# Performance work log

Measured on AMD Instinct MI355X. Metric: run time of the kernel, lower is better.

The kernel has to match this reference:

```python
import jax, jax.numpy as jnp
import numpy as np

HALF = 24576          # per-side HalfKP features (64 king sq * 6 piece * 64 sq)
NUMEL = 2 * HALF      # util.half_kp_numel()
BASE = 128
B = 8192


def _linear(x, W, b):
    return x @ W.T + b


def setup_inputs() -> dict:
    key = jax.random.key(0)
    ks = jax.random.split(key, 16)
    s = 0.01
    return {
        "pov": jax.random.uniform(ks[0], (B, 1), dtype=jnp.float32),
        "white": jax.random.uniform(ks[1], (B, HALF), dtype=jnp.float32),
        "black": jax.random.uniform(ks[2], (B, HALF), dtype=jnp.float32),
        "w_aff_W": jax.random.normal(ks[3], (BASE, NUMEL), dtype=jnp.float32) * s,
        "w_aff_b": jax.random.normal(ks[4], (BASE,), dtype=jnp.float32) * s,
        "b_aff_W": jax.random.normal(ks[5], (BASE, NUMEL), dtype=jnp.float32) * s,
        "b_aff_b": jax.random.normal(ks[6], (BASE,), dtype=jnp.float32) * s,
        "fc0_W": jax.random.normal(ks[7], (32, 2 * BASE), dtype=jnp.float32) * s,
        "fc0_b": jax.random.normal(ks[8], (32,), dtype=jnp.float32) * s,
        "fc1_W": jax.random.normal(ks[9], (32, 32), dtype=jnp.float32) * s,
        "fc1_b": jax.random.normal(ks[10], (32,), dtype=jnp.float32) * s,
        "fc2_W": jax.random.normal(ks[11], (32, 64), dtype=jnp.float32) * s,
        "fc2_b": jax.random.normal(ks[12], (32,), dtype=jnp.float32) * s,
        "fc3_W": jax.random.normal(ks[13], (1, 96), dtype=jnp.float32) * s,
        "fc3_b": jax.random.normal(ks[14], (1,), dtype=jnp.float32) * s,
    }


def reference(pov, white, black, w_aff_W, w_aff_b, b_aff_W, b_aff_b,
              fc0_W, fc0_b, fc1_W, fc1_b, fc2_W, fc2_b, fc3_W, fc3_b):
    # util.half_kp(a, b) = cat([a, b], dim=1)
    w_feat = jnp.concatenate([white, black], axis=1)  # [B, NUMEL]
    b_feat = jnp.concatenate([black, white], axis=1)
    w_ = _linear(w_feat, w_aff_W, w_aff_b)            # [B, 128]
    b_ = _linear(b_feat, b_aff_W, b_aff_b)
    wb = jnp.concatenate([w_, b_], axis=1)            # [B, 256]
    bw = jnp.concatenate([b_, w_], axis=1)
    base = jax.nn.relu(pov * wb + (1.0 - pov) * bw)
    x = jax.nn.relu(_linear(base, fc0_W, fc0_b))      # [B, 32]
    x = jnp.concatenate([x, jax.nn.relu(_linear(x, fc1_W, fc1_b))], axis=1)  # [B, 64]
    x = jnp.concatenate([x, jax.nn.relu(_linear(x, fc2_W, fc2_b))], axis=1)  # [B, 96]
    return _linear(x, fc3_W, fc3_b)                   # [B, 1]
```

## Files before the change

kernel.cpp:

```cpp
#include <hip/hip_runtime.h>
#include <hip/hip_bf16.h>
#include <stdint.h>

typedef float f32x4 __attribute__((ext_vector_type(4)));
typedef float fvec4 __attribute__((ext_vector_type(4)));
typedef short bf16x8 __attribute__((ext_vector_type(8)));
typedef short bf16x4 __attribute__((ext_vector_type(4)));

#define HALF_K 24576
#define NUMELK 49152
#define BATCH  8192
#define BM 256
#define BN 256
#define BK 64

__device__ __forceinline__ short f2bf(float f) {
  __hip_bfloat16 h = __float2bfloat16(f);
  return __builtin_bit_cast(short, h);
}

__device__ __forceinline__ void gload_lds16(const short* g, short* l) {
  __builtin_amdgcn_global_load_lds(
      (const __attribute__((address_space(1))) unsigned*)g,
      (__attribute__((address_space(3))) unsigned*)l, 16, 0, 0);
}

__global__ __launch_bounds__(256)
void nnue_prep(const float* __restrict__ wW, const float* __restrict__ bW,
               short* __restrict__ Bprep) {
  int gid = blockIdx.x * 256 + threadIdx.x;
  int KT  = gid >> 11;
  int rem = gid & 2047;
  int col = rem >> 3;
  int kc  = rem & 7;
  int kg  = KT * 64 + kc * 8;
  const float* src;
  if (col < 128) {
    src = wW + (size_t)col * NUMELK + kg;
  } else {
    int kk = (kg < HALF_K) ? (kg + HALF_K) : (kg - HALF_K);
    src = bW + (size_t)(col - 128) * NUMELK + kk;
  }
  fvec4 v0 = ((const fvec4*)src)[0];
  fvec4 v1 = ((const fvec4*)src)[1];
  bf16x8 o;
  o[0] = f2bf(v0[0]); o[1] = f2bf(v0[1]); o[2] = f2bf(v0[2]); o[3] = f2bf(v0[3]);
  o[4] = f2bf(v1[0]); o[5] = f2bf(v1[1]); o[6] = f2bf(v1[2]); o[7] = f2bf(v1[3]);
  *(bf16x8*)(Bprep + (size_t)KT * 16384 + col * 64 + ((kc ^ (col & 7)) << 3)) = o;
}

__global__ __launch_bounds__(512, 1)
void nnue_gemm(const float* __restrict__ white, const float* __restrict__ black,
               const short* __restrict__ Bprep, float* __restrict__ partial,
               int kchunk, int S) {
  __shared__ short Alds[2][BM * BK];
  __shared__ short Blds[2][BN * BK];

  const int t    = threadIdx.x;
  const int lane = t & 63;
  const int wid  = t >> 6;

  const int bid = blockIdx.x;
  const int xcd = bid & 7, i = bid >> 3;
  const int xpk = 8 / S;
  const int ks  = xcd / xpk;
  const int mt  = (xcd % xpk) * (32 / xpk) + i;
  const int m0  = mt * BM;
  const int k0  = ks * kchunk;
  const int KT0 = k0 / BK;

  f32x4 acc[8][4];
  const f32x4 zero = {0.f, 0.f, 0.f, 0.f};
#pragma unroll
  for (int a = 0; a < 8; ++a)
#pragma unroll
    for (int b = 0; b < 4; ++b) acc[a][b] = zero;

  const int wm = wid >> 2, wn = wid & 3;
  const int l15 = lane & 15, l4 = lane >> 4;

  const int rbase = t >> 4;
  const int cchunk = t & 15;
  const size_t a_off = (size_t)(m0 + rbase) * HALF_K + cchunk * 4;
  const int swz = ((cchunk >> 1) ^ (rbase & 7)) << 3;
  const int halfsh = (cchunk & 1) * 4;

  fvec4 va[8];

  auto issueA = [&](int kg) {
    const float* A; int ka;
    if (kg < HALF_K) { A = white; ka = kg; } else { A = black; ka = kg - HALF_K; }
    const float* base = A + a_off + ka;
#pragma unroll
    for (int j = 0; j < 8; ++j)
      va[j] = *(const fvec4*)(base + (size_t)32 * j * HALF_K);
  };

  auto issueB = [&](int kt_glob, int buf) {
    const short* src = Bprep + (size_t)kt_glob * (BN * BK) + wid * 2048 + lane * 8;
    short* dst = &Blds[buf][wid * 2048];
#pragma unroll
    for (int j = 0; j < 4; ++j)
      gload_lds16(src + j * 512, dst + j * 512);
  };

  auto writeA = [&](int buf) {
#pragma unroll
    for (int j = 0; j < 8; ++j) {
      int row = 32 * j + rbase;
      bf16x4 o;
      o[0] = f2bf(va[j][0]); o[1] = f2bf(va[j][1]);
      o[2] = f2bf(va[j][2]); o[3] = f2bf(va[j][3]);
      *(bf16x4*)&Alds[buf][row * 64 + swz + halfsh] = o;
    }
  };

  const int niter = kchunk / BK;

  issueB(KT0, 0);
  issueA(k0);
  writeA(0);
  __syncthreads();

  for (int kt = 0; kt < niter; ++kt) {
    const int cur = kt & 1;
    const bool hn = (kt + 1 < niter);
    if (hn) {
      issueB(KT0 + kt + 1, cur ^ 1);
      issueA(k0 + (kt + 1) * BK);
    }

    const short* Ab = Alds[cur];
    const short* Bb = Blds[cur];
#pragma unroll
    for (int kstep = 0; kstep < 2; ++kstep) {
      const int kc = kstep * 4 + l4;
      bf16x8 bfr[4];
#pragma unroll
      for (int nf = 0; nf < 4; ++nf) {
        int col = wn * 64 + nf * 16 + l15;
        bfr[nf] = *(const bf16x8*)&Bb[col * 64 + ((kc ^ (col & 7)) << 3)];
      }
#pragma unroll
      for (int mf = 0; mf < 8; ++mf) {
        int row = wm * 128 + mf * 16 + l15;
        bf16x8 af = *(const bf16x8*)&Ab[row * 64 + ((kc ^ (row & 7)) << 3)];
#pragma unroll
        for (int nf = 0; nf < 4; ++nf)
          acc[mf][nf] = __builtin_amdgcn_mfma_f32_16x16x32_bf16(af, bfr[nf], acc[mf][nf], 0, 0, 0);
      }
    }

    if (hn) writeA(cur ^ 1);
    __syncthreads();
  }

  float* P = partial + ((size_t)ks * BATCH + m0) * 256;
#pragma unroll
  for (int mf = 0; mf < 8; ++mf) {
    int row = wm * 128 + mf * 16 + l4 * 4;
#pragma unroll
    for (int nf = 0; nf < 4; ++nf) {
      int col = wn * 64 + nf * 16 + l15;
#pragma unroll
      for (int rr = 0; rr < 4; ++rr)
        P[(size_t)(row + rr) * 256 + col] = acc[mf][nf][rr];
    }
  }
}

__global__ __launch_bounds__(256)
void nnue_tail(const float* __restrict__ partial, int S,
               const float* __restrict__ pov,
               const float* __restrict__ waffb, const float* __restrict__ baffb,
               const float* __restrict__ fc0W, const float* __restrict__ fc0b,
               const float* __restrict__ fc1W, const float* __restrict__ fc1b,
               const float* __restrict__ fc2W, const float* __restrict__ fc2b,
               const float* __restrict__ fc3W, const float* __restrict__ fc3b,
               float* __restrict__ out) {
  __shared__ float w0s[32 * 256];
  __shared__ float w1s[32 * 32];
  __shared__ float w2s[32 * 64];
  __shared__ float w3s[96];
  __shared__ float b0s[32], b1s[32], b2s[32];
  __shared__ float base_s[4][256];
  __shared__ float b3s;

  const int t = threadIdx.x;
  for (int i = t; i < 8192; i += 256) { int j = i >> 8, k = i & 255; w0s[(j << 8) | ((k + j) & 255)] = fc0W[i]; }
  for (int i = t; i < 1024; i += 256) { int j = i >> 5, k = i & 31;  w1s[(j << 5) | ((k + j) & 31)]  = fc1W[i]; }
  for (int i = t; i < 2048; i += 256) { int j = i >> 6, k = i & 63;  w2s[(j << 6) | ((k + j) & 63)]  = fc2W[i]; }
  if (t < 96) w3s[t] = fc3W[t];
  if (t < 32) { b0s[t] = fc0b[t]; b1s[t] = fc1b[t]; b2s[t] = fc2b[t]; }
  if (t == 0) b3s = fc3b[0];
  __syncthreads();

  const int wid = t >> 6, lane = t & 63;
  const int m = blockIdx.x * 4 + wid;
  const float pv = pov[m];

  float val[4];
  {
    const float* p = partial + (size_t)m * 256 + lane * 4;
    fvec4 a = *(const fvec4*)p;
    for (int s = 1; s < S; ++s) a += *(const fvec4*)(p + (size_t)s * BATCH * 256);
    const int c0 = lane * 4;
#pragma unroll
    for (int j = 0; j < 4; ++j) {
      int c = c0 + j;
      float bias = (c < 128) ? waffb[c] : baffb[c - 128];
      val[j] = a[j] + bias;
    }
  }
#pragma unroll
  for (int j = 0; j < 4; ++j) {
    float other = __shfl(val[j], lane ^ 32, 64);
    if (lane < 32) {
      int c = lane * 4 + j;
      float w = val[j], b = other;
      base_s[wid][c]       = fmaxf(pv * w + (1.f - pv) * b, 0.f);
      base_s[wid][c + 128] = fmaxf(pv * b + (1.f - pv) * w, 0.f);
    }
  }
  __syncthreads();

  const int j = lane & 31, half = lane >> 5;
  const float* bs = &base_s[wid][0];

  float s0 = 0.f;
  for (int k = 0; k < 128; ++k) {
    int kk = half * 128 + k;
    s0 += bs[kk] * w0s[(j << 8) | ((kk + j) & 255)];
  }
  s0 += __shfl(s0, lane ^ 32, 64);
  float x0 = fmaxf(s0 + b0s[j], 0.f);

  float s1 = 0.f;
  for (int k = 0; k < 32; ++k)
    s1 += __shfl(x0, k, 64) * w1s[(j << 5) | ((k + j) & 31)];
  float x1 = fmaxf(s1 + b1s[j], 0.f);

  float s2 = 0.f;
  for (int k = 0; k < 32; ++k) {
    s2 += __shfl(x0, k, 64) * w2s[(j << 6) | ((k + j) & 63)];
    s2 += __shfl(x1, k, 64) * w2s[(j << 6) | ((k + 32 + j) & 63)];
  }
  float x2 = fmaxf(s2 + b2s[j], 0.f);

  float s3 = 0.f;
  for (int k = 0; k < 32; ++k) {
    s3 += __shfl(x0, k, 64) * w3s[k];
    s3 += __shfl(x1, k, 64) * w3s[32 + k];
    s3 += __shfl(x2, k, 64) * w3s[64 + k];
  }
  if (lane == 0) out[m] = s3 + b3s;
}

extern "C" void kernel_launch(void* const* d_in, const int* in_sizes, int n_in,
                              void* d_out, int out_size, void* d_ws, size_t ws_size,
                              hipStream_t stream) {
  const float* pov   = (const float*)d_in[0];
  const float* white = (const float*)d_in[1];
  const float* black = (const float*)d_in[2];
  const float* wW    = (const float*)d_in[3];
  const float* wb    = (const float*)d_in[4];
  const float* bW    = (const float*)d_in[5];
  const float* bb    = (const float*)d_in[6];
  const float* fc0W  = (const float*)d_in[7];
  const float* fc0b  = (const float*)d_in[8];
  const float* fc1W  = (const float*)d_in[9];
  const float* fc1b  = (const float*)d_in[10];
  const float* fc2W  = (const float*)d_in[11];
  const float* fc2b  = (const float*)d_in[12];
  const float* fc3W  = (const float*)d_in[13];
  const float* fc3b  = (const float*)d_in[14];
  float* out = (float*)d_out;

  short* Bprep = (short*)d_ws;
  const size_t BWS_BYTES = (size_t)256 * NUMELK * 2;
  float* partial = (float*)((char*)d_ws + BWS_BYTES);
  const size_t PART1 = (size_t)BATCH * 256 * 4;

  int S = 8;
  if (ws_size < BWS_BYTES + 8 * PART1) S = 4;
  if (ws_size < BWS_BYTES + 4 * PART1) S = 2;
  if (ws_size < BWS_BYTES + 2 * PART1) S = 1;

  nnue_prep<<<dim3(6144), 256, 0, stream>>>(wW, bW, Bprep);
  nnue_gemm<<<dim3(32 * S), 512, 0, stream>>>(white, black, Bprep, partial, NUMELK / S, S);
  nnue_tail<<<dim3(BATCH / 4), 256, 0, stream>>>(partial, S, pov, wb, bb,
      fc0W, fc0b, fc1W, fc1b, fc2W, fc2b, fc3W, fc3b, out);
}
```

Measured before the change: 447.1 us.

## Halve GEMM M-tile and restructure pipeline with manual waitcnt and barriers

Shrinks the GEMM M tile from 256 to 128 rows and doubles the grid, so more workgroups are resident per CU. LDS is reorganised to a double-buffered A tile and a single-buffered B tile. The usual __syncthreads are replaced by hand-placed s_waitcnt, s_barrier, sched_barrier and s_setprio, so the next A global loads overlap the MFMA work. In exchange the B weights are re-read by twice as many blocks. The vmcnt accounting is delicate: the global_load_lds traffic for B may not be fully waited on before B is used, which risks a race.

```diff
diff --git a/kernel.cpp b/kernel.cpp
--- a/kernel.cpp
+++ b/kernel.cpp
@@ -10,7 +10,7 @@
 #define HALF_K 24576
 #define NUMELK 49152
 #define BATCH  8192
-#define BM 256
+#define BM 128
 #define BN 256
 #define BK 64
 
@@ -49,89 +49,74 @@
   *(bf16x8*)(Bprep + (size_t)KT * 16384 + col * 64 + ((kc ^ (col & 7)) << 3)) = o;
 }
 
-__global__ __launch_bounds__(512, 1)
+__global__ __launch_bounds__(512, 4)
 void nnue_gemm(const float* __restrict__ white, const float* __restrict__ black,
                const short* __restrict__ Bprep, float* __restrict__ partial,
                int kchunk, int S) {
-  __shared__ short Alds[2][BM * BK];
-  __shared__ short Blds[2][BN * BK];
+  __shared__ short A0s[BM * BK];
+  __shared__ short A1s[BM * BK];
+  __shared__ short Bls[BN * BK];
 
   const int t    = threadIdx.x;
   const int lane = t & 63;
   const int wid  = t >> 6;
 
   const int bid = blockIdx.x;
-  const int xcd = bid & 7, i = bid >> 3;
+  const int xcd = bid & 7, bi = bid >> 3;
   const int xpk = 8 / S;
   const int ks  = xcd / xpk;
-  const int mt  = (xcd % xpk) * (32 / xpk) + i;
+  const int mt  = (xcd % xpk) * (64 / xpk) + bi;
   const int m0  = mt * BM;
   const int k0  = ks * kchunk;
   const int KT0 = k0 / BK;
 
-  f32x4 acc[8][4];
+  f32x4 acc[4][4];
   const f32x4 zero = {0.f, 0.f, 0.f, 0.f};
 #pragma unroll
-  for (int a = 0; a < 8; ++a)
+  for (int a = 0; a < 4; ++a)
 #pragma unroll
     for (int b = 0; b < 4; ++b) acc[a][b] = zero;
 
   const int wm = wid >> 2, wn = wid & 3;
   const int l15 = lane & 15, l4 = lane >> 4;
 
-  const int rbase = t >> 4;
+  const int rbase  = t >> 4;
   const int cchunk = t & 15;
   const size_t a_off = (size_t)(m0 + rbase) * HALF_K + cchunk * 4;
-  const int swz = ((cchunk >> 1) ^ (rbase & 7)) << 3;
+  const int swz    = ((cchunk >> 1) ^ (rbase & 7)) << 3;
   const int halfsh = (cchunk & 1) * 4;
 
-  fvec4 va[8];
+  fvec4 va[4];
 
   auto issueA = [&](int kg) {
-    const float* A; int ka;
-    if (kg < HALF_K) { A = white; ka = kg; } else { A = black; ka = kg - HALF_K; }
-    const float* base = A + a_off + ka;
-#pragma unroll
-    for (int j = 0; j < 8; ++j)
+    const float* Af; int ka;
+    if (kg < HALF_K) { Af = white; ka = kg; } else { Af = black; ka = kg - HALF_K; }
+    const float* base = Af + a_off + ka;
+#pragma unroll
+    for (int j = 0; j < 4; ++j)
       va[j] = *(const fvec4*)(base + (size_t)32 * j * HALF_K);
   };
 
-  auto issueB = [&](int kt_glob, int buf) {
-    const short* src = Bprep + (size_t)kt_glob * (BN * BK) + wid * 2048 + lane * 8;
-    short* dst = &Blds[buf][wid * 2048];
+  auto issueB = [&](int KT) {
+    const short* src = Bprep + (size_t)KT * 16384 + wid * 2048 + lane * 8;
+    short* dst = &Bls[wid * 2048];
 #pragma unroll
     for (int j = 0; j < 4; ++j)
       gload_lds16(src + j * 512, dst + j * 512);
   };
 
-  auto writeA = [&](int buf) {
-#pragma unroll
-    for (int j = 0; j < 8; ++j) {
+  auto writeA = [&](short* Ad) {
+#pragma unroll
+    for (int j = 0; j < 4; ++j) {
       int row = 32 * j + rbase;
       bf16x4 o;
       o[0] = f2bf(va[j][0]); o[1] = f2bf(va[j][1]);
       o[2] = f2bf(va[j][2]); o[3] = f2bf(va[j][3]);
-      *(bf16x4*)&Alds[buf][row * 64 + swz + halfsh] = o;
+      *(bf16x4*)&Ad[row * 64 + swz + halfsh] = o;
     }
   };
 
-  const int niter = kchunk / BK;
-
-  issueB(KT0, 0);
-  issueA(k0);
-  writeA(0);
-  __syncthreads();
-
-  for (int kt = 0; kt < niter; ++kt) {
-    const int cur = kt & 1;
-    const bool hn = (kt + 1 < niter);
-    if (hn) {
-      issueB(KT0 + kt + 1, cur ^ 1);
-      issueA(k0 + (kt + 1) * BK);
-    }
-
-    const short* Ab = Alds[cur];
-    const short* Bb = Blds[cur];
+  auto compute = [&](const short* Ab) {
 #pragma unroll
     for (int kstep = 0; kstep < 2; ++kstep) {
       const int kc = kstep * 4 + l4;
@@ -139,26 +124,58 @@
 #pragma unroll
       for (int nf = 0; nf < 4; ++nf) {
         int col = wn * 64 + nf * 16 + l15;
-        bfr[nf] = *(const bf16x8*)&Bb[col * 64 + ((kc ^ (col & 7)) << 3)];
+        bfr[nf] = *(const bf16x8*)&Bls[col * 64 + ((kc ^ (col & 7)) << 3)];
       }
 #pragma unroll
-      for (int mf = 0; mf < 8; ++mf) {
-        int row = wm * 128 + mf * 16 + l15;
+      for (int mf = 0; mf < 4; ++mf) {
+        int row = wm * 64 + mf * 16 + l15;
         bf16x8 af = *(const bf16x8*)&Ab[row * 64 + ((kc ^ (row & 7)) << 3)];
 #pragma unroll
         for (int nf = 0; nf < 4; ++nf)
           acc[mf][nf] = __builtin_amdgcn_mfma_f32_16x16x32_bf16(af, bfr[nf], acc[mf][nf], 0, 0, 0);
       }
     }
-
-    if (hn) writeA(cur ^ 1);
-    __syncthreads();
+  };
+
+  const int niter = kchunk / BK;
+
+  issueA(k0);
+  issueB(KT0);
+  writeA(A0s);
+  asm volatile("s_waitcnt lgkmcnt(0)" ::: "memory");
+
+  for (int kt = 0; kt < niter; ++kt) {
+    const bool hn = (kt + 1 < niter);
+    short* Acur = (kt & 1) ? A1s : A0s;
+    short* Anxt = (kt & 1) ? A0s : A1s;
+
+    if (hn) {
+      issueA(k0 + (kt + 1) * BK);
+      asm volatile("s_waitcnt vmcnt(8)" ::: "memory");
+    } else {
+      asm volatile("s_waitcnt vmcnt(0)" ::: "memory");
+    }
+    __builtin_amdgcn_sched_barrier(0);
+    __builtin_amdgcn_s_barrier();
+    __builtin_amdgcn_sched_barrier(0);
+
+    __builtin_amdgcn_s_setprio(1);
+    compute(Acur);
+    __builtin_amdgcn_s_setprio(0);
+
+    __builtin_amdgcn_sched_barrier(0);
+    __builtin_amdgcn_s_barrier();
+    if (hn) {
+      issueB(KT0 + kt + 1);
+      writeA(Anxt);
+      asm volatile("s_waitcnt lgkmcnt(0)" ::: "memory");
+    }
   }
 
   float* P = partial + ((size_t)ks * BATCH + m0) * 256;
 #pragma unroll
-  for (int mf = 0; mf < 8; ++mf) {
-    int row = wm * 128 + mf * 16 + l4 * 4;
+  for (int mf = 0; mf < 4; ++mf) {
+    int row = wm * 64 + mf * 16 + l4 * 4;
 #pragma unroll
     for (int nf = 0; nf < 4; ++nf) {
       int col = wn * 64 + nf * 16 + l15;
@@ -287,7 +304,7 @@
   if (ws_size < BWS_BYTES + 2 * PART1) S = 1;
 
   nnue_prep<<<dim3(6144), 256, 0, stream>>>(wW, bW, Bprep);
-  nnue_gemm<<<dim3(32 * S), 512, 0, stream>>>(white, black, Bprep, partial, NUMELK / S, S);
+  nnue_gemm<<<dim3(64 * S), 512, 0, stream>>>(white, black, Bprep, partial, NUMELK / S, S);
   nnue_tail<<<dim3(BATCH / 4), 256, 0, stream>>>(partial, S, pov, wb, bb,
       fc0W, fc0b, fc1W, fc1b, fc2W, fc2b, fc3W, fc3b, out);
 }
```

Result: no change. 445.6 us (-0.4%).
